# Performance work log

Hardware: AMD Instinct MI355X
Metric: run time of the kernel (lower is better)

The kernel has to match this reference:

```python
import jax, jax.numpy as jnp
import numpy as np

G, N, H, OUT, L = 16, 96, 128, 1, 3
DEG = 16
E = G * N * DEG


def setup_inputs() -> dict:
    key = jax.random.key(0)
    ks = iter(jax.random.split(key, 64))
    x = jax.random.randint(next(ks), (G * N, 9), 0, 2)
    edge_attr = jax.random.randint(next(ks), (E, 3), 0, 2)
    # edges grouped per graph (matches PyG batching); global node ids
    edge_graph = jnp.repeat(jnp.arange(G), E // G)
    edge_src = edge_graph * N + jax.random.randint(next(ks), (E,), 0, N)
    edge_dst = edge_graph * N + jax.random.randint(next(ks), (E,), 0, N)

    def lin(shape, fan_in):
        return jax.random.normal(next(ks), shape, jnp.float32) / np.sqrt(fan_in)

    return dict(
        x=x, edge_attr=edge_attr, edge_src=edge_src, edge_dst=edge_dst,
        num_graphs=G, max_nodes=N,
        atom_tables=jax.random.normal(next(ks), (9, 119, H)) * 0.02,
        bond_tables=jax.random.normal(next(ks), (3, 6, H)) * 0.02,
        W_m1=lin((L, 2, 2 * H, H), 2 * H), b_m1=jnp.zeros((L, 2, H)),
        W_m2=lin((L, 2, 2 * H, H), 2 * H), b_m2=jnp.zeros((L, 2, H)),
        W_me=lin((L, 2, H, H), H), b_me=jnp.zeros((L, 2, H)),
        W_mg=lin((L, 2, H, H), H), b_mg=jnp.zeros((L, 2, H)),
        W_mlp1=lin((L, 2, H, H), H), b_mlp1=jnp.zeros((L, 2, H)),
        W_mlp2=lin((L, 2, H, H), H), b_mlp2=jnp.zeros((L, 2, H)),
        W_o1=lin((L, 2, 2 * H, H), 2 * H), b_o1=jnp.zeros((L, 2, H)),
        W_o2=lin((L, 2, H, H), H), b_o2=jnp.zeros((L, 2, H)),
        ln_g=jnp.ones((L, 2, H)), ln_b=jnp.zeros((L, 2, H)),
        W_red=lin((L, 2 * H, H), 2 * H), b_red=jnp.zeros((L, H)),
        W_p1=lin((H, H), H), b_p1=jnp.zeros((H,)),
        W_p2=lin((H, OUT), H), b_p2=jnp.zeros((OUT,)),
    )


def _forward(x, edge_attr, edge_src, edge_dst, num_graphs, max_nodes,
             atom_tables, bond_tables, W_m1, b_m1, W_m2, b_m2, W_me, b_me,
             W_mg, b_mg, W_mlp1, b_mlp1, W_mlp2, b_mlp2, W_o1, b_o1,
             W_o2, b_o2, ln_g, ln_b, W_red, b_red, W_p1, b_p1, W_p2, b_p2):
    Hd = atom_tables.shape[-1]
    # OGB encoders: sum of per-column embeddings
    node_fts = atom_tables[jnp.arange(9)[:, None], x.T].sum(0)          # [G*N, H]
    edge_fts = bond_tables[jnp.arange(3)[:, None], edge_attr.T].sum(0)  # [E, H]
    node = node_fts.reshape(num_graphs, max_nodes, Hd)                  # to_dense_batch (equal-size graphs)
    # per-graph localization of global edge ids (== subtracting per-graph min)
    g = edge_src // max_nodes
    li = edge_src % max_nodes
    lj = edge_dst % max_nodes
    edge_dense = jnp.zeros((num_graphs, max_nodes, max_nodes, Hd),
                           node.dtype).at[g, li, lj].set(edge_fts)      # [G,N,N,H]
    graph_fts = jnp.zeros((num_graphs, Hd), node.dtype)
    hidden = jnp.zeros_like(node)
    for i in range(W_m1.shape[0]):
        outs = []
        for s in range(2):  # random / pretrained streams
            z = jnp.concatenate([node, hidden], -1)                     # [G,N,2H]
            msg1 = z @ W_m1[i, s] + b_m1[i, s]                          # [G,N,H]
            msg2 = z @ W_m2[i, s] + b_m2[i, s]
            msge = edge_dense @ W_me[i, s] + b_me[i, s]                 # [G,N,N,H]
            msgg = graph_fts @ W_mg[i, s] + b_mg[i, s]                  # [G,H]
            msgs = (msg1[:, None, :, :] + msg2[:, :, None, :]
                    + msge + msgg[:, None, None, :])
            m = jax.nn.relu(msgs)
            m = jax.nn.relu(m @ W_mlp1[i, s] + b_mlp1[i, s])
            msgs = m @ W_mlp2[i, s] + b_mlp2[i, s]
            # adj_mat is all ones -> masked max reduces to plain max over senders
            msgs = msgs.max(axis=1)                                     # [G,N,H]
            ret = z @ W_o1[i, s] + b_o1[i, s] + msgs @ W_o2[i, s] + b_o2[i, s]
            ret = jax.nn.relu(ret)
            mu = ret.mean(-1, keepdims=True)
            var = jnp.mean((ret - mu) ** 2, -1, keepdims=True)
            ret = (ret - mu) / jnp.sqrt(var + 1e-5) * ln_g[i, s] + ln_b[i, s]
            outs.append(ret)
        hidden = jnp.concatenate(outs, -1) @ W_red[i] + b_red[i]
    emb = hidden.mean(1)                                                # [G,H]
    h = jax.nn.relu(emb @ W_p1 + b_p1)
    return h @ W_p2 + b_p2                                              # [G,OUT]


def reference(x, edge_attr, edge_src, edge_dst, num_graphs, max_nodes,
              atom_tables, bond_tables, W_m1, b_m1, W_m2, b_m2, W_me, b_me,
              W_mg, b_mg, W_mlp1, b_mlp1, W_mlp2, b_mlp2, W_o1, b_o1,
              W_o2, b_o2, ln_g, ln_b, W_red, b_red, W_p1, b_p1, W_p2, b_p2):
    return _forward(x, edge_attr, edge_src, edge_dst, num_graphs, max_nodes,
                    atom_tables, bond_tables, W_m1, b_m1, W_m2, b_m2, W_me, b_me,
                    W_mg, b_mg, W_mlp1, b_mlp1, W_mlp2, b_mlp2, W_o1, b_o1,
                    W_o2, b_o2, ln_g, ln_b, W_red, b_red, W_p1, b_p1, W_p2, b_p2)
```

## Files before the change

kernel.cpp:

```cpp
#include <hip/hip_runtime.h>
#include <cstddef>

typedef _Float16 f16;
typedef f16 f16x8 __attribute__((ext_vector_type(8)));
typedef float f32x4 __attribute__((ext_vector_type(4)));

constexpr int NG    = 16;
constexpr int NNODE = 96;
constexpr int TOTN  = 1536;
constexpr int HD    = 128;
constexpr int NEDGE = 24576;
constexpr int NLAY  = 3;
constexpr int PSTR  = 17;

__device__ __forceinline__ f32x4 mfma16(f16x8 a, f16x8 b, f32x4 c) {
    return __builtin_amdgcn_mfma_f32_16x16x32_f16(a, b, c, 0, 0, 0);
}

__global__ void k_embed_nodes(const int* x, const float* atab, f16* zA) {
    const int v = blockIdx.x, h = threadIdx.x;
    float s = 0.f;
    for (int c = 0; c < 9; ++c)
        s += atab[((size_t)(c * 119 + x[v * 9 + c])) * HD + h];
    const size_t base = ((size_t)(v >> 4) * 32);
    zA[((base + (h >> 3)) * 16 + (v & 15)) * 8 + (h & 7)] = (f16)s;
    zA[((base + 16 + (h >> 3)) * 16 + (v & 15)) * 8 + (h & 7)] = (f16)0.f;
}

__global__ void k_embed_edges(const int* ea, const float* btab, f16* eftsA) {
    const int e = blockIdx.x, h = threadIdx.x;
    float s = 0.f;
    for (int c = 0; c < 3; ++c)
        s += btab[((size_t)(c * 6 + ea[e * 3 + c])) * HD + h];
    eftsA[(((size_t)(e >> 4) * 16 + (h >> 3)) * 16 + (e & 15)) * 8 + (h & 7)] = (f16)s;
}

__global__ void k_winit(int* winner) {
    winner[blockIdx.x * 256 + threadIdx.x] = -1;
}

__global__ void k_winner(const int* esrc, const int* edst, int* winner) {
    const int e = blockIdx.x * 256 + threadIdx.x;
    const int sg = esrc[e];
    const int g = sg / NNODE;
    const int li = sg - g * NNODE;
    const int lj = edst[e] - g * NNODE;
    atomicMax(&winner[((size_t)g * NNODE + li) * NNODE + lj], e);
}

__global__ void k_wswz(const float* Wm1, const float* Wm2, const float* Wo1,
                       const float* Wred, const float* Wo2, const float* W1,
                       const float* W2, const float* We,
                       f16* sm1, f16* sm2, f16* so1, f16* sred, f16* so2,
                       f16* s1, f16* s2, f16* sme) {
    const int idx = blockIdx.x * 256 + threadIdx.x;
    const int S256 = 6 * 256 * 128;
    const int SRED = 3 * 256 * 128;
    const int S128 = 6 * 128 * 128;
    const float* src;
    f16* dst;
    int rel, sh;
    if (idx < S256)                   { src = Wm1;  dst = sm1;  rel = idx;              sh = 15; }
    else if (idx < 2 * S256)          { src = Wm2;  dst = sm2;  rel = idx - S256;       sh = 15; }
    else if (idx < 3 * S256)          { src = Wo1;  dst = so1;  rel = idx - 2 * S256;   sh = 15; }
    else if (idx < 3 * S256 + SRED)   { src = Wred; dst = sred; rel = idx - 3 * S256;   sh = 15; }
    else if (idx < 3 * S256 + SRED + S128)
        { src = Wo2; dst = so2; rel = idx - 3 * S256 - SRED; sh = 14; }
    else if (idx < 3 * S256 + SRED + 2 * S128)
        { src = W1;  dst = s1;  rel = idx - 3 * S256 - SRED - S128; sh = 14; }
    else if (idx < 3 * S256 + SRED + 3 * S128)
        { src = W2;  dst = s2;  rel = idx - 3 * S256 - SRED - 2 * S128; sh = 14; }
    else if (idx < 3 * S256 + SRED + 4 * S128)
        { src = We;  dst = sme; rel = idx - 3 * S256 - SRED - 3 * S128; sh = 14; }
    else return;
    const int mat = rel >> sh;
    const int r2 = rel & ((1 << sh) - 1);
    const int k = r2 >> 7, n = r2 & 127;
    dst[(size_t)mat * (1 << sh) + (((k >> 3) * 128 + n) << 3) + (k & 7)] = (f16)src[rel];
}

__global__ __launch_bounds__(256) void k_ngemm(
    const f16* __restrict__ zA,
    const f16* __restrict__ sm1, const f16* __restrict__ sm2, const f16* __restrict__ so1,
    const float* __restrict__ bm1, const float* __restrict__ bm2,
    const float* __restrict__ bme, const float* __restrict__ bmg,
    const float* __restrict__ bo1,
    float* __restrict__ msg1, float* __restrict__ msg2, float* __restrict__ o1buf,
    int layer) {
    const int tid = threadIdx.x, lane = tid & 63, w = tid >> 6;
    const int mr = lane & 15, q = lane >> 4;
    const int t0 = blockIdx.x;
    const int wh = blockIdx.y >> 1, s = blockIdx.y & 1, ls = layer * 2 + s;
    const f16* B;
    float* out;
    float bias[8];
    if (wh == 0) {
        B = sm1 + (size_t)ls * 32768; out = msg1 + (size_t)s * TOTN * HD;
        for (int nt = 0; nt < 8; ++nt) {
            const int col = nt * 16 + mr;
            bias[nt] = bm1[ls * HD + col] + bme[ls * HD + col] + bmg[ls * HD + col];
        }
    } else if (wh == 1) {
        B = sm2 + (size_t)ls * 32768; out = msg2 + (size_t)s * TOTN * HD;
        for (int nt = 0; nt < 8; ++nt) bias[nt] = bm2[ls * HD + nt * 16 + mr];
    } else {
        B = so1 + (size_t)ls * 32768; out = o1buf + (size_t)s * TOTN * HD;
        for (int nt = 0; nt < 8; ++nt) bias[nt] = bo1[ls * HD + nt * 16 + mr];
    }
    const size_t tIdx = (size_t)t0 * 4 + w;
    f32x4 acc[8];
#pragma unroll
    for (int nt = 0; nt < 8; ++nt) acc[nt] = (f32x4){0.f, 0.f, 0.f, 0.f};
#pragma unroll
    for (int kt = 0; kt < 8; ++kt) {
        const int kq = kt * 4 + q;
        f16x8 a = *(const f16x8*)&zA[((tIdx * 32 + kq) * 16 + mr) * 8];
        const f16* bp = B + ((size_t)kq * HD) * 8;
#pragma unroll
        for (int nt = 0; nt < 8; ++nt) {
            f16x8 bv = *(const f16x8*)(bp + (nt * 16 + mr) * 8);
            acc[nt] = mfma16(a, bv, acc[nt]);
        }
    }
#pragma unroll
    for (int nt = 0; nt < 8; ++nt) {
        const int col = nt * 16 + mr;
#pragma unroll
        for (int r = 0; r < 4; ++r) {
            const int row = t0 * 64 + w * 16 + q * 4 + r;
            out[(size_t)row * HD + col] = acc[nt][r] + bias[nt];
        }
    }
}

__global__ __launch_bounds__(256) void k_egemm(
    const f16* __restrict__ eftsA, const f16* __restrict__ sme,
    f16* __restrict__ emsg) {
    const int tid = threadIdx.x, lane = tid & 63, w = tid >> 6;
    const int mr = lane & 15, q = lane >> 4;
    const int ls = blockIdx.y;
    const f16* B = sme + (size_t)ls * 16384;
    f32x4 acc[2][8];
#pragma unroll
    for (int mt = 0; mt < 2; ++mt)
#pragma unroll
        for (int nt = 0; nt < 8; ++nt) acc[mt][nt] = (f32x4){0.f, 0.f, 0.f, 0.f};
#pragma unroll
    for (int kt = 0; kt < 4; ++kt) {
        const int kq = kt * 4 + q;
        f16x8 a0 = *(const f16x8*)&eftsA[(((size_t)(blockIdx.x * 8 + 2 * w + 0) * 16 + kq) * 16 + mr) * 8];
        f16x8 a1 = *(const f16x8*)&eftsA[(((size_t)(blockIdx.x * 8 + 2 * w + 1) * 16 + kq) * 16 + mr) * 8];
        const f16* bp = B + ((size_t)kq * HD) * 8;
#pragma unroll
        for (int nt = 0; nt < 8; ++nt) {
            f16x8 bv = *(const f16x8*)(bp + (nt * 16 + mr) * 8);
            acc[0][nt] = mfma16(a0, bv, acc[0][nt]);
            acc[1][nt] = mfma16(a1, bv, acc[1][nt]);
        }
    }
#pragma unroll
    for (int mt = 0; mt < 2; ++mt) {
        const int ebase = blockIdx.x * 128 + (2 * w + mt) * 16 + q * 4;
#pragma unroll
        for (int nt = 0; nt < 8; ++nt) {
            const int col = nt * 16 + mr;
#pragma unroll
            for (int r = 0; r < 4; ++r)
                emsg[((size_t)ls * NEDGE + ebase + r) * HD + col] = (f16)acc[mt][nt][r];
        }
    }
}

__global__ __launch_bounds__(256) void k_pairs(
    const float* __restrict__ msg1, const float* __restrict__ msg2,
    const f16* __restrict__ emsg, const int* __restrict__ winner,
    const f16* __restrict__ w1s, const float* __restrict__ bmlp1,
    const f16* __restrict__ w2s, const float* __restrict__ bmlp2,
    float* __restrict__ maxpart, int layer) {
    __shared__ __align__(16) f16 Pb[((7 * 16 + 15) * PSTR + 15) * 8 + 8];
    __shared__ __align__(16) f16 Qb[((7 * 16 + 15) * PSTR + 15) * 8 + 8];
    const int tid = threadIdx.x, lane = tid & 63, w = tid >> 6;
    const int mr = lane & 15, q = lane >> 4;
    const int jt = blockIdx.x, b = blockIdx.y, zz = blockIdx.z;
    const int cp = zz >> 1, s = zz & 1, ls = layer * 2 + s;
    const int j0 = jt * 16;
    const float* M1 = msg1 + ((size_t)s * TOTN + b * NNODE) * HD;
    const float* M2 = msg2 + ((size_t)s * TOTN + b * NNODE) * HD;
    const f16* EM = emsg + (size_t)ls * NEDGE * HD;
    const f16* W1 = w1s + (size_t)ls * HD * HD;
    const f16* W2 = w2s + (size_t)ls * HD * HD;
    f16x8 Bf1[4][2], Bf2[4][2];
#pragma unroll
    for (int kt = 0; kt < 4; ++kt)
#pragma unroll
        for (int ntl = 0; ntl < 2; ++ntl) {
            const size_t off = ((size_t)(kt * 4 + q) * 128 + (2 * w + ntl) * 16 + mr) * 8;
            Bf1[kt][ntl] = *(const f16x8*)(W1 + off);
            Bf2[kt][ntl] = *(const f16x8*)(W2 + off);
        }
    float b1v[2], b2v[2];
#pragma unroll
    for (int ntl = 0; ntl < 2; ++ntl) {
        const int col = (2 * w + ntl) * 16 + mr;
        b1v[ntl] = bmlp1[ls * HD + col];
        b2v[ntl] = bmlp2[ls * HD + col];
    }
    float maxr[2][4];
#pragma unroll
    for (int ntl = 0; ntl < 2; ++ntl)
#pragma unroll
        for (int r = 0; r < 4; ++r) maxr[ntl][r] = -3.402823466e38f;

    const int prow = tid >> 1, half = tid & 1;
    const int pj = prow & 15, pii = prow >> 4;
    const float* m1r = M1 + (size_t)(j0 + pj) * HD + half * 64;

    for (int it = 0; it < 6; ++it) {
        const int i = cp * 48 + it * 8 + pii;
        {
            const int wv = winner[((size_t)b * NNODE + i) * NNODE + (j0 + pj)];
            const float* m2r = M2 + (size_t)i * HD + half * 64;
            const f16* er = EM + (size_t)(wv < 0 ? 0 : wv) * HD + half * 64;
#pragma unroll
            for (int c8 = 0; c8 < 64; c8 += 8) {
                float4 x0 = *(const float4*)(m1r + c8);
                float4 x1 = *(const float4*)(m1r + c8 + 4);
                float4 y0 = *(const float4*)(m2r + c8);
                float4 y1 = *(const float4*)(m2r + c8 + 4);
                float v[8] = {x0.x + y0.x, x0.y + y0.y, x0.z + y0.z, x0.w + y0.w,
                              x1.x + y1.x, x1.y + y1.y, x1.z + y1.z, x1.w + y1.w};
                if (wv >= 0) {
                    f16x8 e8 = *(const f16x8*)(er + c8);
#pragma unroll
                    for (int u = 0; u < 8; ++u) v[u] += (float)e8[u];
                }
                f16x8 pv;
#pragma unroll
                for (int u = 0; u < 8; ++u) pv[u] = (f16)fmaxf(v[u], 0.f);
                const int k = half * 64 + c8;
                *(f16x8*)&Pb[((pii * 16 + (k >> 3)) * PSTR + pj) * 8] = pv;
            }
        }
        __syncthreads();
        f32x4 acc[8][2];
#pragma unroll
        for (int mt = 0; mt < 8; ++mt)
#pragma unroll
            for (int ntl = 0; ntl < 2; ++ntl) acc[mt][ntl] = (f32x4){0.f, 0.f, 0.f, 0.f};
#pragma unroll
        for (int kt = 0; kt < 4; ++kt) {
#pragma unroll
            for (int mt = 0; mt < 8; ++mt) {
                f16x8 a = *(const f16x8*)&Pb[((mt * 16 + kt * 4 + q) * PSTR + mr) * 8];
                acc[mt][0] = mfma16(a, Bf1[kt][0], acc[mt][0]);
                acc[mt][1] = mfma16(a, Bf1[kt][1], acc[mt][1]);
            }
        }
#pragma unroll
        for (int mt = 0; mt < 8; ++mt)
#pragma unroll
            for (int ntl = 0; ntl < 2; ++ntl) {
                const int col = (2 * w + ntl) * 16 + mr;
                const int kg = col >> 3, kj = col & 7;
#pragma unroll
                for (int r = 0; r < 4; ++r) {
                    float v = fmaxf(acc[mt][ntl][r] + b1v[ntl], 0.f);
                    Qb[((mt * 16 + kg) * PSTR + q * 4 + r) * 8 + kj] = (f16)v;
                }
            }
        __syncthreads();
#pragma unroll
        for (int mt = 0; mt < 8; ++mt)
#pragma unroll
            for (int ntl = 0; ntl < 2; ++ntl) acc[mt][ntl] = (f32x4){0.f, 0.f, 0.f, 0.f};
#pragma unroll
        for (int kt = 0; kt < 4; ++kt) {
#pragma unroll
            for (int mt = 0; mt < 8; ++mt) {
                f16x8 a = *(const f16x8*)&Qb[((mt * 16 + kt * 4 + q) * PSTR + mr) * 8];
                acc[mt][0] = mfma16(a, Bf2[kt][0], acc[mt][0]);
                acc[mt][1] = mfma16(a, Bf2[kt][1], acc[mt][1]);
            }
        }
#pragma unroll
        for (int ntl = 0; ntl < 2; ++ntl)
#pragma unroll
            for (int r = 0; r < 4; ++r) {
                float m0 = acc[0][ntl][r];
#pragma unroll
                for (int mt = 1; mt < 8; ++mt) m0 = fmaxf(m0, acc[mt][ntl][r]);
                maxr[ntl][r] = fmaxf(maxr[ntl][r], m0 + b2v[ntl]);
            }
        __syncthreads();
    }
#pragma unroll
    for (int ntl = 0; ntl < 2; ++ntl) {
        const int col = (2 * w + ntl) * 16 + mr;
#pragma unroll
        for (int r = 0; r < 4; ++r) {
            const int j = j0 + q * 4 + r;
            maxpart[((size_t)zz * TOTN + b * NNODE + j) * HD + col] = maxr[ntl][r];
        }
    }
}

__global__ __launch_bounds__(256) void k_pr(
    const float* __restrict__ maxpart, const float* __restrict__ o1buf,
    const f16* __restrict__ so2, const float* __restrict__ bo2,
    const float* __restrict__ lng, const float* __restrict__ lnb,
    const f16* __restrict__ sred, const float* __restrict__ bred,
    float* __restrict__ hiddenf, f16* __restrict__ zA, int layer) {
    __shared__ __align__(16) f16 Af[16384];
    const int tid = threadIdx.x, lane = tid & 63, w = tid >> 6;
    const int mr = lane & 15, q = lane >> 4;
    const int row0 = blockIdx.x * 64;
    {
        const int mrow = tid >> 1, half = tid & 1;
        const int sb = mrow >> 6, rl = mrow & 63;
        const int row = row0 + rl;
#pragma unroll
        for (int c8 = 0; c8 < 64; c8 += 8) {
            const int col = half * 64 + c8;
            const float* p0 = maxpart + ((size_t)(0 + sb) * TOTN + row) * HD + col;
            const float* p1 = maxpart + ((size_t)(2 + sb) * TOTN + row) * HD + col;
            float4 u0 = *(const float4*)p0;
            float4 u1 = *(const float4*)(p0 + 4);
            float4 v0 = *(const float4*)p1;
            float4 v1 = *(const float4*)(p1 + 4);
            f16x8 pv;
            pv[0] = (f16)fmaxf(u0.x, v0.x); pv[1] = (f16)fmaxf(u0.y, v0.y);
            pv[2] = (f16)fmaxf(u0.z, v0.z); pv[3] = (f16)fmaxf(u0.w, v0.w);
            pv[4] = (f16)fmaxf(u1.x, v1.x); pv[5] = (f16)fmaxf(u1.y, v1.y);
            pv[6] = (f16)fmaxf(u1.z, v1.z); pv[7] = (f16)fmaxf(u1.w, v1.w);
            *(f16x8*)&Af[(((sb * 4 + (rl >> 4)) * 16 + (col >> 3)) * 16 + (rl & 15)) * 8] = pv;
        }
    }
    __syncthreads();
    const int sw = w >> 1, ls = layer * 2 + sw;
    const f16* B1 = so2 + (size_t)ls * 16384;
    f32x4 acc[2][8];
#pragma unroll
    for (int mt = 0; mt < 2; ++mt)
#pragma unroll
        for (int nt = 0; nt < 8; ++nt) acc[mt][nt] = (f32x4){0.f, 0.f, 0.f, 0.f};
#pragma unroll
    for (int kt = 0; kt < 4; ++kt) {
        const int kq = kt * 4 + q;
        f16x8 a0 = *(const f16x8*)&Af[(((sw * 4 + (w & 1) * 2 + 0) * 16 + kq) * 16 + mr) * 8];
        f16x8 a1 = *(const f16x8*)&Af[(((sw * 4 + (w & 1) * 2 + 1) * 16 + kq) * 16 + mr) * 8];
        const f16* bp = B1 + ((size_t)kq * HD) * 8;
#pragma unroll
        for (int nt = 0; nt < 8; ++nt) {
            f16x8 bv = *(const f16x8*)(bp + (nt * 16 + mr) * 8);
            acc[0][nt] = mfma16(a0, bv, acc[0][nt]);
            acc[1][nt] = mfma16(a1, bv, acc[1][nt]);
        }
    }
    float lngv[8], lnbv[8], bo2v[8];
#pragma unroll
    for (int nt = 0; nt < 8; ++nt) {
        const int col = nt * 16 + mr;
        lngv[nt] = lng[ls * HD + col];
        lnbv[nt] = lnb[ls * HD + col];
        bo2v[nt] = bo2[ls * HD + col];
    }
#pragma unroll
    for (int mt = 0; mt < 2; ++mt) {
#pragma unroll
        for (int nt = 0; nt < 8; ++nt) {
            const int col = nt * 16 + mr;
#pragma unroll
            for (int r = 0; r < 4; ++r) {
                const int rl = (w & 1) * 32 + mt * 16 + q * 4 + r;
                float v = acc[mt][nt][r] + bo2v[nt] +
                          o1buf[((size_t)sw * TOTN + row0 + rl) * HD + col];
                acc[mt][nt][r] = fmaxf(v, 0.f);
            }
        }
#pragma unroll
        for (int r = 0; r < 4; ++r) {
            float su = 0.f, sq = 0.f;
#pragma unroll
            for (int nt = 0; nt < 8; ++nt) {
                su += acc[mt][nt][r];
                sq += acc[mt][nt][r] * acc[mt][nt][r];
            }
#pragma unroll
            for (int mask = 1; mask <= 8; mask <<= 1) {
                su += __shfl_xor(su, mask, 64);
                sq += __shfl_xor(sq, mask, 64);
            }
            const float mean = su * (1.f / 128.f);
            float var = sq * (1.f / 128.f) - mean * mean;
            var = fmaxf(var, 0.f);
            const float rstd = 1.f / sqrtf(var + 1e-5f);
#pragma unroll
            for (int nt = 0; nt < 8; ++nt)
                acc[mt][nt][r] = (acc[mt][nt][r] - mean) * rstd * lngv[nt] + lnbv[nt];
        }
    }
    __syncthreads();
#pragma unroll
    for (int mt = 0; mt < 2; ++mt)
#pragma unroll
        for (int nt = 0; nt < 8; ++nt) {
            const int kg2 = sw * 16 + nt * 2 + (mr >> 3), j2 = mr & 7;
#pragma unroll
            for (int r = 0; r < 4; ++r) {
                const int rl = (w & 1) * 32 + mt * 16 + q * 4 + r;
                Af[(((rl >> 4) * 32 + kg2) * 16 + (rl & 15)) * 8 + j2] = (f16)acc[mt][nt][r];
            }
        }
    __syncthreads();
    const f16* B2 = sred + (size_t)layer * 32768;
    f32x4 a2[8];
#pragma unroll
    for (int nt = 0; nt < 8; ++nt) a2[nt] = (f32x4){0.f, 0.f, 0.f, 0.f};
#pragma unroll
    for (int kt = 0; kt < 8; ++kt) {
        const int kq = kt * 4 + q;
        f16x8 av = *(const f16x8*)&Af[((w * 32 + kq) * 16 + mr) * 8];
        const f16* bp = B2 + ((size_t)kq * HD) * 8;
#pragma unroll
        for (int nt = 0; nt < 8; ++nt) {
            f16x8 bv = *(const f16x8*)(bp + (nt * 16 + mr) * 8);
            a2[nt] = mfma16(av, bv, a2[nt]);
        }
    }
#pragma unroll
    for (int nt = 0; nt < 8; ++nt) {
        const int col = nt * 16 + mr;
        const float bb = bred[layer * HD + col];
#pragma unroll
        for (int r = 0; r < 4; ++r) {
            const int row = row0 + w * 16 + q * 4 + r;
            const float v = a2[nt][r] + bb;
            hiddenf[(size_t)row * HD + col] = v;
            zA[(((size_t)(row >> 4) * 32 + 16 + (col >> 3)) * 16 + (row & 15)) * 8 + (col & 7)] = (f16)v;
        }
    }
}

__global__ void k_final(const float* hiddenf, const float* Wp1, const float* bp1,
                        const float* Wp2, const float* bp2, float* out) {
    __shared__ float se[128];
    __shared__ float sr[128];
    const int b = blockIdx.x, h = threadIdx.x;
    float acc = 0.f;
    for (int v = 0; v < NNODE; ++v)
        acc += hiddenf[((size_t)b * NNODE + v) * HD + h];
    se[h] = acc * (1.f / 96.f);
    __syncthreads();
    float a2 = bp1[h];
    for (int k = 0; k < 128; ++k)
        a2 += se[k] * Wp1[(size_t)k * HD + h];
    a2 = fmaxf(a2, 0.f);
    sr[h] = a2 * Wp2[h];
    __syncthreads();
    for (int off = 64; off > 0; off >>= 1) {
        if (h < off) sr[h] += sr[h + off];
        __syncthreads();
    }
    if (h == 0) out[b] = sr[0] + bp2[0];
}

extern "C" void kernel_launch(void* const* d_in, const int* in_sizes, int n_in,
                              void* d_out, int out_size, void* d_ws, size_t ws_size,
                              hipStream_t stream) {
    (void)in_sizes; (void)n_in; (void)out_size; (void)ws_size;
    const int* x    = (const int*)d_in[0];
    const int* ea   = (const int*)d_in[1];
    const int* esrc = (const int*)d_in[2];
    const int* edst = (const int*)d_in[3];
    const float* atab = (const float*)d_in[6];
    const float* btab = (const float*)d_in[7];
    const float* Wm1 = (const float*)d_in[8];    const float* bm1 = (const float*)d_in[9];
    const float* Wm2 = (const float*)d_in[10];   const float* bm2 = (const float*)d_in[11];
    const float* Wme = (const float*)d_in[12];   const float* bme = (const float*)d_in[13];
    const float* bmg = (const float*)d_in[15];
    const float* Wmlp1 = (const float*)d_in[16]; const float* bmlp1 = (const float*)d_in[17];
    const float* Wmlp2 = (const float*)d_in[18]; const float* bmlp2 = (const float*)d_in[19];
    const float* Wo1 = (const float*)d_in[20];   const float* bo1 = (const float*)d_in[21];
    const float* Wo2 = (const float*)d_in[22];   const float* bo2 = (const float*)d_in[23];
    const float* lng = (const float*)d_in[24];   const float* lnb = (const float*)d_in[25];
    const float* Wred = (const float*)d_in[26];  const float* bred = (const float*)d_in[27];
    const float* Wp1 = (const float*)d_in[28];   const float* bp1 = (const float*)d_in[29];
    const float* Wp2 = (const float*)d_in[30];   const float* bp2 = (const float*)d_in[31];

    char* cur = (char*)d_ws;
    f16* zA = (f16*)cur;          cur += (size_t)TOTN * 256 * 2;
    float* hiddenf = (float*)cur; cur += (size_t)TOTN * HD * 4;
    f16* eftsA = (f16*)cur;       cur += (size_t)NEDGE * HD * 2;
    f16* emsg = (f16*)cur;        cur += (size_t)6 * NEDGE * HD * 2;
    float* msg1 = (float*)cur;    cur += (size_t)2 * TOTN * HD * 4;
    float* msg2 = (float*)cur;    cur += (size_t)2 * TOTN * HD * 4;
    float* o1buf = (float*)cur;   cur += (size_t)2 * TOTN * HD * 4;
    float* maxpart = (float*)cur; cur += (size_t)4 * TOTN * HD * 4;
    int* winner = (int*)cur;      cur += (size_t)NG * NNODE * NNODE * 4;
    f16* sw1 = (f16*)cur;         cur += (size_t)6 * HD * HD * 2;
    f16* sw2 = (f16*)cur;         cur += (size_t)6 * HD * HD * 2;
    f16* swme = (f16*)cur;        cur += (size_t)6 * HD * HD * 2;
    f16* swm1 = (f16*)cur;        cur += (size_t)6 * 256 * HD * 2;
    f16* swm2 = (f16*)cur;        cur += (size_t)6 * 256 * HD * 2;
    f16* swo1 = (f16*)cur;        cur += (size_t)6 * 256 * HD * 2;
    f16* swred = (f16*)cur;       cur += (size_t)3 * 256 * HD * 2;
    f16* swo2 = (f16*)cur;        cur += (size_t)6 * HD * HD * 2;

    k_winit<<<(NG * NNODE * NNODE) / 256, 256, 0, stream>>>(winner);
    k_embed_nodes<<<TOTN, 128, 0, stream>>>(x, atab, zA);
    k_embed_edges<<<NEDGE, 128, 0, stream>>>(ea, btab, eftsA);
    k_winner<<<NEDGE / 256, 256, 0, stream>>>(esrc, edst, winner);
    k_wswz<<<4224, 256, 0, stream>>>(Wm1, Wm2, Wo1, Wred, Wo2, Wmlp1, Wmlp2, Wme,
                                     swm1, swm2, swo1, swred, swo2, sw1, sw2, swme);
    k_egemm<<<dim3(192, 6), 256, 0, stream>>>(eftsA, swme, emsg);
    for (int layer = 0; layer < NLAY; ++layer) {
        k_ngemm<<<dim3(24, 6), 256, 0, stream>>>(zA, swm1, swm2, swo1,
                                                 bm1, bm2, bme, bmg, bo1,
                                                 msg1, msg2, o1buf, layer);
        k_pairs<<<dim3(6, NG, 4), 256, 0, stream>>>(msg1, msg2, emsg, winner,
                                                    sw1, bmlp1, sw2, bmlp2,
                                                    maxpart, layer);
        k_pr<<<24, 256, 0, stream>>>(maxpart, o1buf, swo2, bo2, lng, lnb,
                                     swred, bred, hiddenf, zA, layer);
    }
    k_final<<<NG, 128, 0, stream>>>(hiddenf, Wp1, bp1, Wp2, bp2, (float*)d_out);
}
```

Before: 456.8 us.

## Build pair-MLP input directly in registers and split source nodes into more chunks

k_pairs no longer materialises the relu(m1+m2+edge) tile in shared memory. It now caches the msg2 rows for the block in LDS as f16 and keeps msg1 fragments in registers, then forms the MFMA A operand directly in registers, which removes one barrier and one LDS round trip per iteration. The grid doubles along i (8 chunks of 24 nodes), so k_pr reduces over four partial-max buffers instead of two. The add and relu now run in f16 rather than f32, which slightly changes rounding.

```diff
diff --git a/kernel.cpp b/kernel.cpp
--- a/kernel.cpp
+++ b/kernel.cpp
@@ -3,6 +3,7 @@
 
 typedef _Float16 f16;
 typedef f16 f16x8 __attribute__((ext_vector_type(8)));
+typedef f16 f16x4 __attribute__((ext_vector_type(4)));
 typedef float f32x4 __attribute__((ext_vector_type(4)));
 
 constexpr int NG    = 16;
@@ -11,7 +12,6 @@
 constexpr int HD    = 128;
 constexpr int NEDGE = 24576;
 constexpr int NLAY  = 3;
-constexpr int PSTR  = 17;
 
 __device__ __forceinline__ f32x4 mfma16(f16x8 a, f16x8 b, f32x4 c) {
     return __builtin_amdgcn_mfma_f32_16x16x32_f16(a, b, c, 0, 0, 0);
@@ -177,18 +177,36 @@
     const f16* __restrict__ w1s, const float* __restrict__ bmlp1,
     const f16* __restrict__ w2s, const float* __restrict__ bmlp2,
     float* __restrict__ maxpart, int layer) {
-    __shared__ __align__(16) f16 Pb[((7 * 16 + 15) * PSTR + 15) * 8 + 8];
-    __shared__ __align__(16) f16 Qb[((7 * 16 + 15) * PSTR + 15) * 8 + 8];
+    __shared__ __align__(16) f16 M2s[24 * 128];
+    __shared__ __align__(16) f16 Qb[128 * 128];
     const int tid = threadIdx.x, lane = tid & 63, w = tid >> 6;
     const int mr = lane & 15, q = lane >> 4;
     const int jt = blockIdx.x, b = blockIdx.y, zz = blockIdx.z;
     const int cp = zz >> 1, s = zz & 1, ls = layer * 2 + s;
-    const int j0 = jt * 16;
-    const float* M1 = msg1 + ((size_t)s * TOTN + b * NNODE) * HD;
-    const float* M2 = msg2 + ((size_t)s * TOTN + b * NNODE) * HD;
+    const int j0 = jt * 16, i0 = cp * 24;
     const f16* EM = emsg + (size_t)ls * NEDGE * HD;
     const f16* W1 = w1s + (size_t)ls * HD * HD;
     const f16* W2 = w2s + (size_t)ls * HD * HD;
+    for (int idx = tid * 4; idx < 24 * 128; idx += 1024) {
+        const int row = idx >> 7, col = idx & 127;
+        float4 v = *(const float4*)&msg2[((size_t)s * TOTN + b * NNODE + i0 + row) * HD + col];
+        f16x4 h;
+        h[0] = (f16)v.x; h[1] = (f16)v.y; h[2] = (f16)v.z; h[3] = (f16)v.w;
+        *(f16x4*)&M2s[idx] = h;
+    }
+    f16x8 m1f[4];
+    {
+        const float* m1p = msg1 + ((size_t)s * TOTN + b * NNODE + j0 + mr) * HD;
+#pragma unroll
+        for (int kt = 0; kt < 4; ++kt) {
+            float4 p0 = *(const float4*)(m1p + kt * 32 + q * 8);
+            float4 p1 = *(const float4*)(m1p + kt * 32 + q * 8 + 4);
+            m1f[kt][0] = (f16)p0.x; m1f[kt][1] = (f16)p0.y;
+            m1f[kt][2] = (f16)p0.z; m1f[kt][3] = (f16)p0.w;
+            m1f[kt][4] = (f16)p1.x; m1f[kt][5] = (f16)p1.y;
+            m1f[kt][6] = (f16)p1.z; m1f[kt][7] = (f16)p1.w;
+        }
+    }
     f16x8 Bf1[4][2], Bf2[4][2];
 #pragma unroll
     for (int kt = 0; kt < 4; ++kt)
@@ -210,50 +228,35 @@
     for (int ntl = 0; ntl < 2; ++ntl)
 #pragma unroll
         for (int r = 0; r < 4; ++r) maxr[ntl][r] = -3.402823466e38f;
-
-    const int prow = tid >> 1, half = tid & 1;
-    const int pj = prow & 15, pii = prow >> 4;
-    const float* m1r = M1 + (size_t)(j0 + pj) * HD + half * 64;
-
-    for (int it = 0; it < 6; ++it) {
-        const int i = cp * 48 + it * 8 + pii;
-        {
-            const int wv = winner[((size_t)b * NNODE + i) * NNODE + (j0 + pj)];
-            const float* m2r = M2 + (size_t)i * HD + half * 64;
-            const f16* er = EM + (size_t)(wv < 0 ? 0 : wv) * HD + half * 64;
-#pragma unroll
-            for (int c8 = 0; c8 < 64; c8 += 8) {
-                float4 x0 = *(const float4*)(m1r + c8);
-                float4 x1 = *(const float4*)(m1r + c8 + 4);
-                float4 y0 = *(const float4*)(m2r + c8);
-                float4 y1 = *(const float4*)(m2r + c8 + 4);
-                float v[8] = {x0.x + y0.x, x0.y + y0.y, x0.z + y0.z, x0.w + y0.w,
-                              x1.x + y1.x, x1.y + y1.y, x1.z + y1.z, x1.w + y1.w};
-                if (wv >= 0) {
-                    f16x8 e8 = *(const f16x8*)(er + c8);
-#pragma unroll
-                    for (int u = 0; u < 8; ++u) v[u] += (float)e8[u];
+    __syncthreads();
+
+    for (int it = 0; it < 3; ++it) {
+        const int ibase = i0 + it * 8;
+        int wv[8];
+#pragma unroll
+        for (int mt = 0; mt < 8; ++mt)
+            wv[mt] = winner[((size_t)b * NNODE + ibase + mt) * NNODE + j0 + mr];
+        f32x4 acc[8][2];
+#pragma unroll
+        for (int mt = 0; mt < 8; ++mt)
+#pragma unroll
+            for (int ntl = 0; ntl < 2; ++ntl) acc[mt][ntl] = (f32x4){0.f, 0.f, 0.f, 0.f};
+#pragma unroll
+        for (int kt = 0; kt < 4; ++kt) {
+            const int ko = kt * 32 + q * 8;
+#pragma unroll
+            for (int mt = 0; mt < 8; ++mt) {
+                f16x8 m2v = *(const f16x8*)&M2s[(it * 8 + mt) * 128 + ko];
+                f16x8 av = m1f[kt] + m2v;
+                if (wv[mt] >= 0) {
+                    f16x8 ev = *(const f16x8*)&EM[(size_t)wv[mt] * HD + ko];
+                    av = av + ev;
                 }
-                f16x8 pv;
-#pragma unroll
-                for (int u = 0; u < 8; ++u) pv[u] = (f16)fmaxf(v[u], 0.f);
-                const int k = half * 64 + c8;
-                *(f16x8*)&Pb[((pii * 16 + (k >> 3)) * PSTR + pj) * 8] = pv;
-            }
-        }
-        __syncthreads();
-        f32x4 acc[8][2];
-#pragma unroll
-        for (int mt = 0; mt < 8; ++mt)
-#pragma unroll
-            for (int ntl = 0; ntl < 2; ++ntl) acc[mt][ntl] = (f32x4){0.f, 0.f, 0.f, 0.f};
-#pragma unroll
-        for (int kt = 0; kt < 4; ++kt) {
-#pragma unroll
-            for (int mt = 0; mt < 8; ++mt) {
-                f16x8 a = *(const f16x8*)&Pb[((mt * 16 + kt * 4 + q) * PSTR + mr) * 8];
-                acc[mt][0] = mfma16(a, Bf1[kt][0], acc[mt][0]);
-                acc[mt][1] = mfma16(a, Bf1[kt][1], acc[mt][1]);
+#pragma unroll
+                for (int u = 0; u < 8; ++u)
+                    av[u] = av[u] > (f16)0.f ? av[u] : (f16)0.f;
+                acc[mt][0] = mfma16(av, Bf1[kt][0], acc[mt][0]);
+                acc[mt][1] = mfma16(av, Bf1[kt][1], acc[mt][1]);
             }
         }
 #pragma unroll
@@ -265,7 +268,7 @@
 #pragma unroll
                 for (int r = 0; r < 4; ++r) {
                     float v = fmaxf(acc[mt][ntl][r] + b1v[ntl], 0.f);
-                    Qb[((mt * 16 + kg) * PSTR + q * 4 + r) * 8 + kj] = (f16)v;
+                    Qb[((mt * 16 + kg) * 16 + q * 4 + r) * 8 + kj] = (f16)v;
                 }
             }
         __syncthreads();
@@ -277,7 +280,7 @@
         for (int kt = 0; kt < 4; ++kt) {
 #pragma unroll
             for (int mt = 0; mt < 8; ++mt) {
-                f16x8 a = *(const f16x8*)&Qb[((mt * 16 + kt * 4 + q) * PSTR + mr) * 8];
+                f16x8 a = *(const f16x8*)&Qb[((mt * 16 + kt * 4 + q) * 16 + mr) * 8];
                 acc[mt][0] = mfma16(a, Bf2[kt][0], acc[mt][0]);
                 acc[mt][1] = mfma16(a, Bf2[kt][1], acc[mt][1]);
             }
@@ -321,17 +324,21 @@
 #pragma unroll
         for (int c8 = 0; c8 < 64; c8 += 8) {
             const int col = half * 64 + c8;
-            const float* p0 = maxpart + ((size_t)(0 + sb) * TOTN + row) * HD + col;
-            const float* p1 = maxpart + ((size_t)(2 + sb) * TOTN + row) * HD + col;
-            float4 u0 = *(const float4*)p0;
-            float4 u1 = *(const float4*)(p0 + 4);
-            float4 v0 = *(const float4*)p1;
-            float4 v1 = *(const float4*)(p1 + 4);
+            float mx[8] = {-3.4e38f, -3.4e38f, -3.4e38f, -3.4e38f,
+                           -3.4e38f, -3.4e38f, -3.4e38f, -3.4e38f};
+#pragma unroll
+            for (int ch = 0; ch < 4; ++ch) {
+                const float* p = maxpart + ((size_t)(ch * 2 + sb) * TOTN + row) * HD + col;
+                float4 u0 = *(const float4*)p;
+                float4 u1 = *(const float4*)(p + 4);
+                mx[0] = fmaxf(mx[0], u0.x); mx[1] = fmaxf(mx[1], u0.y);
+                mx[2] = fmaxf(mx[2], u0.z); mx[3] = fmaxf(mx[3], u0.w);
+                mx[4] = fmaxf(mx[4], u1.x); mx[5] = fmaxf(mx[5], u1.y);
+                mx[6] = fmaxf(mx[6], u1.z); mx[7] = fmaxf(mx[7], u1.w);
+            }
             f16x8 pv;
-            pv[0] = (f16)fmaxf(u0.x, v0.x); pv[1] = (f16)fmaxf(u0.y, v0.y);
-            pv[2] = (f16)fmaxf(u0.z, v0.z); pv[3] = (f16)fmaxf(u0.w, v0.w);
-            pv[4] = (f16)fmaxf(u1.x, v1.x); pv[5] = (f16)fmaxf(u1.y, v1.y);
-            pv[6] = (f16)fmaxf(u1.z, v1.z); pv[7] = (f16)fmaxf(u1.w, v1.w);
+#pragma unroll
+            for (int u = 0; u < 8; ++u) pv[u] = (f16)mx[u];
             *(f16x8*)&Af[(((sb * 4 + (rl >> 4)) * 16 + (col >> 3)) * 16 + (rl & 15)) * 8] = pv;
         }
     }
@@ -495,7 +502,7 @@
     float* msg1 = (float*)cur;    cur += (size_t)2 * TOTN * HD * 4;
     float* msg2 = (float*)cur;    cur += (size_t)2 * TOTN * HD * 4;
     float* o1buf = (float*)cur;   cur += (size_t)2 * TOTN * HD * 4;
-    float* maxpart = (float*)cur; cur += (size_t)4 * TOTN * HD * 4;
+    float* maxpart = (float*)cur; cur += (size_t)8 * TOTN * HD * 4;
     int* winner = (int*)cur;      cur += (size_t)NG * NNODE * NNODE * 4;
     f16* sw1 = (f16*)cur;         cur += (size_t)6 * HD * HD * 2;
     f16* sw2 = (f16*)cur;         cur += (size_t)6 * HD * HD * 2;
@@ -517,7 +524,7 @@
         k_ngemm<<<dim3(24, 6), 256, 0, stream>>>(zA, swm1, swm2, swo1,
                                                  bm1, bm2, bme, bmg, bo1,
                                                  msg1, msg2, o1buf, layer);
-        k_pairs<<<dim3(6, NG, 4), 256, 0, stream>>>(msg1, msg2, emsg, winner,
+        k_pairs<<<dim3(6, NG, 8), 256, 0, stream>>>(msg1, msg2, emsg, winner,
                                                     sw1, bmlp1, sw2, bmlp2,
                                                     maxpart, layer);
         k_pr<<<24, 256, 0, stream>>>(maxpart, o1buf, swo2, bo2, lng, lnb,
```

New measurement: 472.4 us. 3.4% more time.
